# Kernel tuning notes

Measured on AMD Instinct MI355X. Metric: run time of the kernel, lower is better.

The kernel has to match this reference:

```python
import jax, jax.numpy as jnp
import numpy as np

N = 100_000      # nodes
E = 1_600_000    # directed input edges (no self loops, unique canonical pairs)
F_IN = 256       # num_features
HID = 128        # 2 * num_hidden (GATConv out width)
NHID = 64        # num_hidden
C = 4            # num_classes
G = 128          # number of graphs in the batch
NEG_SLOPE = 0.2  # PyG GATConv default LeakyReLU slope


def setup_inputs() -> dict:
    key = jax.random.key(0)
    ks = jax.random.split(key, 16)

    # --- graph structure (numpy; deduped canonical pairs so that
    # concat(e, reversed(e)) exactly matches PyG to_undirected+coalesce) ---
    rng = np.random.RandomState(0)
    n_cand = int(E * 1.05)
    s = rng.randint(0, N, size=n_cand)
    off = rng.randint(1, N, size=n_cand)
    d = (s + off) % N                      # guarantees no self loops
    lo, hi = np.minimum(s, d), np.maximum(s, d)
    pairs = np.unique(lo.astype(np.int64) * N + hi.astype(np.int64))[:E]
    src = (pairs // N).astype(np.int64)
    dst = (pairs % N).astype(np.int64)
    edge_index = jnp.asarray(np.stack([src, dst]))  # [2, E]

    batch = jnp.sort(jax.random.randint(ks[0], (N,), 0, G)).astype(jnp.int64)
    x = jax.random.normal(ks[1], (N, F_IN), dtype=jnp.float32)

    sc = 0.05
    params = dict(
        W1=jax.random.normal(ks[2], (HID, F_IN)) * sc,
        as1=jax.random.normal(ks[3], (HID,)) * sc,
        ad1=jax.random.normal(ks[4], (HID,)) * sc,
        b1=jnp.zeros((HID,), jnp.float32),
        W2=jax.random.normal(ks[5], (HID, HID)) * sc,
        as2=jax.random.normal(ks[6], (HID,)) * sc,
        ad2=jax.random.normal(ks[7], (HID,)) * sc,
        b2=jnp.zeros((HID,), jnp.float32),
        fw1=jax.random.normal(ks[8], (NHID, HID)) * sc,
        fb1=jnp.zeros((NHID,), jnp.float32),
        fw2=jax.random.normal(ks[9], (C, NHID)) * sc,
        fb2=jnp.zeros((C,), jnp.float32),
    )
    return dict(x=x, edge_index=edge_index, batch=batch, **params)


def _gat_conv(h_in, src, dst, W, a_src, a_dst, bias):
    """PyG GATConv, heads=1, concat=True. src/dst include self loops."""
    h = h_in @ W.T                                        # [N, out]
    # per-edge attention logits: a_src . h_j + a_dst . h_i
    e = jax.nn.leaky_relu((h @ a_src)[src] + (h @ a_dst)[dst], NEG_SLOPE)
    # edge softmax over incoming edges of each dst node
    m = jax.ops.segment_max(e, dst, num_segments=N)       # [N]
    w = jnp.exp(e - m[dst])
    denom = jax.ops.segment_sum(w, dst, num_segments=N)   # [N] (>0: self loops)
    alpha = w / denom[dst]                                # [Etot]
    out = jax.ops.segment_sum(h[src] * alpha[:, None], dst, num_segments=N)
    return out + bias


def reference(x, edge_index, batch,
              W1, as1, ad1, b1, W2, as2, ad2, b2,
              fw1, fb1, fw2, fb2):
    # to_undirected: input has unique canonical (lo<hi) pairs -> concat exact
    s0, d0 = edge_index[0], edge_index[1]
    loop = jnp.arange(N, dtype=s0.dtype)
    src = jnp.concatenate([s0, d0, loop])  # GATConv adds self loops
    dst = jnp.concatenate([d0, s0, loop])

    h = jax.nn.selu(_gat_conv(x, src, dst, W1, as1, ad1, b1))
    h = jax.nn.selu(_gat_conv(h, src, dst, W2, as2, ad2, b2))

    # global mean pool over graphs
    sums = jax.ops.segment_sum(h, batch, num_segments=G)            # [G, HID]
    cnt = jax.ops.segment_sum(jnp.ones((N,), h.dtype), batch, num_segments=G)
    g = jax.nn.selu(sums / jnp.maximum(cnt, 1.0)[:, None])

    g = jax.nn.selu(g @ fw1.T + fb1)
    # dropout p=0.5 is identity in eval mode
    logits = g @ fw2.T + fb2
    return jax.nn.log_softmax(logits, axis=-1)                      # [G, C]
```

## Files before the change

kernel.cpp:

```cpp
#include <hip/hip_runtime.h>
#include <hip/hip_bf16.h>


#define NN 100000
#define EE 1600000
#define GG 128
#define HID 128
#define AGG_CAP 512
#define NEG_SLOPE 0.2f

typedef short bf16x8 __attribute__((ext_vector_type(8)));
typedef float f32x4 __attribute__((ext_vector_type(4)));

__device__ __forceinline__ float lrelu(float x) { return x > 0.f ? x : NEG_SLOPE * x; }

__device__ __forceinline__ float selu(float x) {
    const float sc = 1.0507009873554805f, al = 1.6732632423543772f;
    return x > 0.f ? sc * x : sc * al * (__expf(x) - 1.f);
}

__device__ __forceinline__ unsigned short f2bf(float x) {
    unsigned int b = __float_as_uint(x);
    b += 0x7FFFu + ((b >> 16) & 1u);
    return (unsigned short)(b >> 16);
}


__global__ __launch_bounds__(256) void castbf_kernel(const float* __restrict__ in,
                                                     unsigned short* __restrict__ out, int n) {
    int i = (blockIdx.x * blockDim.x + threadIdx.x) * 4;
    if (i >= n) return;
    float4 v = *reinterpret_cast<const float4*>(in + i);
    union { unsigned short u[4]; uint2 w; } pk;
    pk.u[0] = f2bf(v.x); pk.u[1] = f2bf(v.y); pk.u[2] = f2bf(v.z); pk.u[3] = f2bf(v.w);
    *reinterpret_cast<uint2*>(out + i) = pk.w;
}


__global__ __launch_bounds__(256) void loptr_kernel(const int* __restrict__ ei,
                                                    int* __restrict__ loptr, int n, int E_) {
    int v = blockIdx.x * blockDim.x + threadIdx.x;
    if (v > n) return;
    int lo = 0, hi = E_;
    while (lo < hi) {
        int mid = (lo + hi) >> 1;
        if (ei[mid] < v) lo = mid + 1; else hi = mid;
    }
    loptr[v] = lo;
}


__global__ void count_kernel(const int* __restrict__ ei, int* __restrict__ deg, int E_) {
    int e = blockIdx.x * blockDim.x + threadIdx.x;
    if (e >= E_) return;
    atomicAdd(&deg[ei[E_ + e]], 1);
}

#define SCAN_CHUNK 512

__global__ __launch_bounds__(256) void block_sum_kernel(const int* __restrict__ deg,
                                                        int* __restrict__ bsum, int n) {
    __shared__ int sd[256];
    int b = blockIdx.x, t = threadIdx.x;
    int base = b * SCAN_CHUNK;
    int v = 0;
    int i0 = base + t, i1 = base + t + 256;
    if (i0 < n) v += deg[i0];
    if (i1 < n) v += deg[i1];
    sd[t] = v;
    __syncthreads();
    for (int off = 128; off; off >>= 1) {
        if (t < off) sd[t] += sd[t + off];
        __syncthreads();
    }
    if (t == 0) bsum[b] = sd[0];
}

__global__ __launch_bounds__(256) void top_scan_kernel(const int* __restrict__ bsum,
                                                       int* __restrict__ boff, int nb,
                                                       int* __restrict__ total_out) {
    __shared__ int a[256], b[256];
    int t = threadIdx.x;
    int v = (t < nb) ? bsum[t] : 0;
    int* cur = a; int* nxt = b;
    cur[t] = v;
    __syncthreads();
    for (int off = 1; off < 256; off <<= 1) {
        int val = cur[t] + ((t >= off) ? cur[t - off] : 0);
        nxt[t] = val;
        __syncthreads();
        int* tmp = cur; cur = nxt; nxt = tmp;
    }
    if (t < nb) boff[t] = cur[t] - v;
    if (t == nb - 1) *total_out = cur[t];
}

__global__ __launch_bounds__(512) void scan_final_kernel(const int* __restrict__ deg,
                                                         const int* __restrict__ boff,
                                                         int* __restrict__ row_ptr,
                                                         int* __restrict__ cursor, int n) {
    __shared__ int a[512], b[512];
    int blk = blockIdx.x, t = threadIdx.x;
    int i = blk * 512 + t;
    int v = (i < n) ? deg[i] : 0;
    int orig = v;
    int* cur = a; int* nxt = b;
    cur[t] = v;
    __syncthreads();
    for (int off = 1; off < 512; off <<= 1) {
        int val = cur[t] + ((t >= off) ? cur[t - off] : 0);
        nxt[t] = val;
        __syncthreads();
        int* tmp = cur; cur = nxt; nxt = tmp;
    }
    if (i < n) {
        int excl = cur[t] - orig + boff[blk];
        row_ptr[i] = excl;
        cursor[i] = excl;
    }
}

__global__ void scatter_kernel(const int* __restrict__ ei, int* __restrict__ cursor,
                               int* __restrict__ csr, int E_) {
    int e = blockIdx.x * blockDim.x + threadIdx.x;
    if (e >= E_) return;
    int u = ei[e], v = ei[E_ + e];
    int p = atomicAdd(&cursor[v], 1);
    csr[p] = u;
}


template<int K, bool BF16IN>
__global__ __launch_bounds__(256) void mfma_gemm(const void* __restrict__ Ain,
                                                 const unsigned short* __restrict__ Wb,
                                                 const float* __restrict__ avs,
                                                 const float* __restrict__ avd,
                                                 unsigned short* __restrict__ Cb,
                                                 float* __restrict__ hs,
                                                 float* __restrict__ hd,
                                                 int M) {
    __shared__ unsigned short As[128 * 32];
    __shared__ unsigned short Bs[128 * 32];
    __shared__ float hsp[128][2];
    __shared__ float hdp[128][2];
    int tid = threadIdx.x;
    int brow = blockIdx.x * 128;
    int w = tid >> 6, lane = tid & 63;
    int wr = (w >> 1) * 64, wc = (w & 1) * 64;
    int whalf = w & 1;
    int l15 = lane & 15, g = lane >> 4;

    const f32x4 zero = {0.f, 0.f, 0.f, 0.f};
    f32x4 acc[4][4];
    #pragma unroll
    for (int m = 0; m < 4; ++m)
        #pragma unroll
        for (int n = 0; n < 4; ++n) acc[m][n] = zero;

    int srow = tid >> 2;
    int slot = tid & 3;

    for (int k0 = 0; k0 < K; k0 += 32) {
        #pragma unroll
        for (int half = 0; half < 2; ++half) {
            int r = srow + half * 64;
            int grow = brow + r;
            union { unsigned short u[8]; uint4 v; } pk;
            if (BF16IN) {
                const unsigned short* A16 = (const unsigned short*)Ain;
                if (grow < M)
                    pk.v = *reinterpret_cast<const uint4*>(A16 + (size_t)grow * K + k0 + slot * 8);
                else pk.v = make_uint4(0, 0, 0, 0);
            } else {
                const float* A32 = (const float*)Ain;
                if (grow < M) {
                    const float4* p = reinterpret_cast<const float4*>(A32 + (size_t)grow * K + k0 + slot * 8);
                    float4 f0 = p[0], f1 = p[1];
                    pk.u[0] = f2bf(f0.x); pk.u[1] = f2bf(f0.y);
                    pk.u[2] = f2bf(f0.z); pk.u[3] = f2bf(f0.w);
                    pk.u[4] = f2bf(f1.x); pk.u[5] = f2bf(f1.y);
                    pk.u[6] = f2bf(f1.z); pk.u[7] = f2bf(f1.w);
                } else pk.v = make_uint4(0, 0, 0, 0);
            }
            int ss = slot ^ (r & 3);
            *reinterpret_cast<uint4*>(&As[r * 32 + ss * 8]) = pk.v;
        }
        #pragma unroll
        for (int half = 0; half < 2; ++half) {
            int r = srow + half * 64;
            uint4 v = *reinterpret_cast<const uint4*>(Wb + (size_t)r * K + k0 + slot * 8);
            int ss = slot ^ (r & 3);
            *reinterpret_cast<uint4*>(&Bs[r * 32 + ss * 8]) = v;
        }
        __syncthreads();

        bf16x8 af[4], bfr[4];
        #pragma unroll
        for (int m = 0; m < 4; ++m) {
            int row = wr + m * 16 + l15;
            af[m] = *reinterpret_cast<const bf16x8*>(&As[row * 32 + ((g ^ (row & 3)) * 8)]);
        }
        #pragma unroll
        for (int n = 0; n < 4; ++n) {
            int col = wc + n * 16 + l15;
            bfr[n] = *reinterpret_cast<const bf16x8*>(&Bs[col * 32 + ((g ^ (col & 3)) * 8)]);
        }
        #pragma unroll
        for (int m = 0; m < 4; ++m)
            #pragma unroll
            for (int n = 0; n < 4; ++n)
                acc[m][n] = __builtin_amdgcn_mfma_f32_16x16x32_bf16(af[m], bfr[n], acc[m][n], 0, 0, 0);
        __syncthreads();
    }

    #pragma unroll
    for (int m = 0; m < 4; ++m) {
        int rbase = brow + wr + m * 16 + g * 4;
        #pragma unroll
        for (int j = 0; j < 4; ++j) {
            int row = rbase + j;
            if (row < M) {
                #pragma unroll
                for (int n = 0; n < 4; ++n) {
                    int col = wc + n * 16 + l15;
                    Cb[(size_t)row * 128 + col] = f2bf(acc[m][n][j]);
                }
            }
        }
    }

    float asv[4], adv[4];
    #pragma unroll
    for (int n = 0; n < 4; ++n) {
        asv[n] = avs[wc + n * 16 + l15];
        adv[n] = avd[wc + n * 16 + l15];
    }
    #pragma unroll
    for (int m = 0; m < 4; ++m) {
        #pragma unroll
        for (int j = 0; j < 4; ++j) {
            float vs = 0.f, vd = 0.f;
            #pragma unroll
            for (int n = 0; n < 4; ++n) {
                float a = acc[m][n][j];
                vs = fmaf(a, asv[n], vs);
                vd = fmaf(a, adv[n], vd);
            }
            #pragma unroll
            for (int off = 1; off < 16; off <<= 1) {
                vs += __shfl_xor(vs, off);
                vd += __shfl_xor(vd, off);
            }
            if (l15 == 0) {
                int rl = wr + m * 16 + g * 4 + j;
                hsp[rl][whalf] = vs;
                hdp[rl][whalf] = vd;
            }
        }
    }
    __syncthreads();
    if (tid < 128) {
        int row = brow + tid;
        if (row < M) {
            hs[row] = hsp[tid][0] + hsp[tid][1];
            hd[row] = hdp[tid][0] + hdp[tid][1];
        }
    }
}


__global__ __launch_bounds__(256) void agg_kernel(const unsigned int* __restrict__ hb32,
                                                  const float* __restrict__ hs,
                                                  const float* __restrict__ hd,
                                                  const int* __restrict__ loptr,
                                                  const int* __restrict__ eiD,
                                                  const int* __restrict__ hiptr,
                                                  const int* __restrict__ csr,
                                                  const float* __restrict__ bias,
                                                  unsigned int* __restrict__ outb,
                                                  int n) {
    __shared__ float esh[4][AGG_CAP];
    __shared__ int ush[4][AGG_CAP];
    int wib = threadIdx.x >> 6;
    int lane = threadIdx.x & 63;
    int v = blockIdx.x * 4 + wib;
    if (v >= n) return;
    int s_lo = loptr[v];
    int dlo = loptr[v + 1] - s_lo;
    int s_hi = hiptr[v];
    int d = dlo + (hiptr[v + 1] - s_hi);
    float hdv = hd[v];
    float e_self = lrelu(hs[v] + hdv);
    float m, inv;
    bool fits = (d <= AGG_CAP);

    auto nbr = [&](int k) -> int {
        return (k < dlo) ? eiD[s_lo + k] : csr[s_hi + k - dlo];
    };
    auto gx = [&](int u) -> float2 {
        unsigned int w = hb32[(size_t)u * 64 + lane];
        return make_float2(__uint_as_float(w << 16), __uint_as_float(w & 0xFFFF0000u));
    };

    if (fits) {
        float mloc = -3.4e38f;
        for (int k = lane; k < d; k += 64) {
            int u = nbr(k);
            float e = lrelu(hs[u] + hdv);
            ush[wib][k] = u;
            esh[wib][k] = e;
            mloc = fmaxf(mloc, e);
        }
        #pragma unroll
        for (int off = 32; off; off >>= 1) mloc = fmaxf(mloc, __shfl_xor(mloc, off));
        m = fmaxf(mloc, e_self);
        float sloc = 0.f;
        for (int k = lane; k < d; k += 64) sloc += __expf(esh[wib][k] - m);
        #pragma unroll
        for (int off = 32; off; off >>= 1) sloc += __shfl_xor(sloc, off);
        float s = sloc + __expf(e_self - m);
        inv = 1.f / s;
        for (int k = lane; k < d; k += 64) esh[wib][k] = __expf(esh[wib][k] - m) * inv;
    } else {
        float mloc = -3.4e38f;
        for (int k = lane; k < d; k += 64) mloc = fmaxf(mloc, lrelu(hs[nbr(k)] + hdv));
        #pragma unroll
        for (int off = 32; off; off >>= 1) mloc = fmaxf(mloc, __shfl_xor(mloc, off));
        m = fmaxf(mloc, e_self);
        float sloc = 0.f;
        for (int k = lane; k < d; k += 64) sloc += __expf(lrelu(hs[nbr(k)] + hdv) - m);
        #pragma unroll
        for (int off = 32; off; off >>= 1) sloc += __shfl_xor(sloc, off);
        float s = sloc + __expf(e_self - m);
        inv = 1.f / s;
    }
    __syncthreads();

    float2 hvv = gx(v);
    float a_self = __expf(e_self - m) * inv;
    float accx = a_self * hvv.x;
    float accy = a_self * hvv.y;
    if (fits) {
        int k = 0;
        for (; k + 8 <= d; k += 8) {
            float a_[8]; int u_[8]; float2 x_[8];
            #pragma unroll
            for (int j = 0; j < 8; ++j) { a_[j] = esh[wib][k + j]; u_[j] = ush[wib][k + j]; }
            #pragma unroll
            for (int j = 0; j < 8; ++j) x_[j] = gx(u_[j]);
            #pragma unroll
            for (int j = 0; j < 8; ++j) {
                accx = fmaf(a_[j], x_[j].x, accx);
                accy = fmaf(a_[j], x_[j].y, accy);
            }
        }
        for (; k < d; ++k) {
            float al = esh[wib][k];
            float2 xv = gx(ush[wib][k]);
            accx = fmaf(al, xv.x, accx);
            accy = fmaf(al, xv.y, accy);
        }
    } else {
        for (int k = 0; k < d; ++k) {
            int u = nbr(k);
            float al = __expf(lrelu(hs[u] + hdv) - m) * inv;
            float2 xv = gx(u);
            accx = fmaf(al, xv.x, accx);
            accy = fmaf(al, xv.y, accy);
        }
    }
    float2 bb = reinterpret_cast<const float2*>(bias)[lane];
    float o0 = selu(accx + bb.x);
    float o1 = selu(accy + bb.y);
    unsigned int pb = ((unsigned int)f2bf(o1) << 16) | (unsigned int)f2bf(o0);
    outb[(size_t)v * 64 + lane] = pb;
}


__device__ __forceinline__ int lower_bound_dev(const int* __restrict__ b, int n, int val) {
    int lo = 0, hi = n;
    while (lo < hi) {
        int mid = (lo + hi) >> 1;
        if (b[mid] < val) lo = mid + 1; else hi = mid;
    }
    return lo;
}

__global__ __launch_bounds__(1024) void pool_mlp_kernel(const unsigned int* __restrict__ hb,
                                                        const int* __restrict__ batch,
                                                        const float* __restrict__ fw1,
                                                        const float* __restrict__ fb1,
                                                        const float* __restrict__ fw2,
                                                        const float* __restrict__ fb2,
                                                        float* __restrict__ out, int n) {
    int g = blockIdx.x;
    int t = threadIdx.x;
    int lane = t & 63;
    int rg = t >> 6;
    __shared__ float2 sm[16][64];
    __shared__ float gv[128];
    __shared__ float hid[64];
    __shared__ float logits[4];

    int s = lower_bound_dev(batch, n, g);
    int e = lower_bound_dev(batch, n, g + 1);

    float2 acc = make_float2(0.f, 0.f);
    int i = s + rg;
    for (; i + 16 < e; i += 32) {
        unsigned int w0 = hb[(size_t)i * 64 + lane];
        unsigned int w1 = hb[(size_t)(i + 16) * 64 + lane];
        acc.x += __uint_as_float(w0 << 16) + __uint_as_float(w1 << 16);
        acc.y += __uint_as_float(w0 & 0xFFFF0000u) + __uint_as_float(w1 & 0xFFFF0000u);
    }
    for (; i < e; i += 16) {
        unsigned int w0 = hb[(size_t)i * 64 + lane];
        acc.x += __uint_as_float(w0 << 16);
        acc.y += __uint_as_float(w0 & 0xFFFF0000u);
    }
    sm[rg][lane] = acc;
    __syncthreads();
    if (rg == 0) {
        float2 tot = make_float2(0.f, 0.f);
        #pragma unroll
        for (int r = 0; r < 16; ++r) {
            tot.x += sm[r][lane].x;
            tot.y += sm[r][lane].y;
        }
        float cnt = fmaxf((float)(e - s), 1.0f);
        gv[lane * 2 + 0] = selu(tot.x / cnt);
        gv[lane * 2 + 1] = selu(tot.y / cnt);
    }
    __syncthreads();
    if (t < 64) {
        float a = fb1[t];
        for (int k = 0; k < 128; ++k) a = fmaf(fw1[t * 128 + k], gv[k], a);
        hid[t] = selu(a);
    }
    __syncthreads();
    if (t < 4) {
        float a = fb2[t];
        for (int k = 0; k < 64; ++k) a = fmaf(fw2[t * 64 + k], hid[k], a);
        logits[t] = a;
    }
    __syncthreads();
    if (t < 4) {
        float mx = fmaxf(fmaxf(logits[0], logits[1]), fmaxf(logits[2], logits[3]));
        float sum = __expf(logits[0] - mx) + __expf(logits[1] - mx) +
                    __expf(logits[2] - mx) + __expf(logits[3] - mx);
        out[g * 4 + t] = logits[t] - mx - logf(sum);
    }
}


extern "C" void kernel_launch(void* const* d_in, const int* in_sizes, int n_in,
                              void* d_out, int out_size, void* d_ws, size_t ws_size,
                              hipStream_t stream) {
    const float* x   = (const float*)d_in[0];
    const int*   ei  = (const int*)d_in[1];
    const int*   bat = (const int*)d_in[2];
    const float* W1  = (const float*)d_in[3];
    const float* as1 = (const float*)d_in[4];
    const float* ad1 = (const float*)d_in[5];
    const float* b1  = (const float*)d_in[6];
    const float* W2  = (const float*)d_in[7];
    const float* as2 = (const float*)d_in[8];
    const float* ad2 = (const float*)d_in[9];
    const float* b2  = (const float*)d_in[10];
    const float* fw1 = (const float*)d_in[11];
    const float* fb1 = (const float*)d_in[12];
    const float* fw2 = (const float*)d_in[13];
    const float* fb2 = (const float*)d_in[14];
    float* out = (float*)d_out;

    char* ws = (char*)d_ws;
    size_t off = 0;
    auto alloc = [&](size_t bytes) {
        void* p = ws + off;
        off += (bytes + 255) & ~(size_t)255;
        return p;
    };
    unsigned short* hb      = (unsigned short*)alloc((size_t)NN * 128 * 2);
    unsigned short* hbB     = (unsigned short*)alloc((size_t)NN * 128 * 2);
    unsigned short* wb1     = (unsigned short*)alloc((size_t)HID * 256 * 2);
    unsigned short* wb2     = (unsigned short*)alloc((size_t)HID * 128 * 2);
    float*          hs      = (float*)alloc((size_t)NN * 4);
    float*          hd      = (float*)alloc((size_t)NN * 4);
    int*            deg     = (int*)alloc((size_t)NN * 4);
    int*            row_ptr = (int*)alloc((size_t)(NN + 1) * 4);
    int*            cursor  = (int*)alloc((size_t)NN * 4);
    int*            loptr   = (int*)alloc((size_t)(NN + 1) * 4);
    int*            csr     = (int*)alloc((size_t)EE * 4);
    int*            bsum    = (int*)alloc(256 * 4);
    int*            boff    = (int*)alloc(256 * 4);

    hipMemsetAsync(deg, 0, (size_t)NN * 4, stream);
    loptr_kernel<<<(NN + 1 + 255) / 256, 256, 0, stream>>>(ei, loptr, NN, EE);
    count_kernel<<<(EE + 255) / 256, 256, 0, stream>>>(ei, deg, EE);
    int NB = (NN + SCAN_CHUNK - 1) / SCAN_CHUNK;
    block_sum_kernel<<<NB, 256, 0, stream>>>(deg, bsum, NN);
    top_scan_kernel<<<1, 256, 0, stream>>>(bsum, boff, NB, row_ptr + NN);
    scan_final_kernel<<<NB, 512, 0, stream>>>(deg, boff, row_ptr, cursor, NN);
    scatter_kernel<<<(EE + 255) / 256, 256, 0, stream>>>(ei, cursor, csr, EE);

    castbf_kernel<<<(HID * 256 / 4 + 255) / 256, 256, 0, stream>>>(W1, wb1, HID * 256);
    castbf_kernel<<<(HID * 128 / 4 + 255) / 256, 256, 0, stream>>>(W2, wb2, HID * 128);

    const int* eiD = ei + EE;
    int gemmGrid = (NN + 127) / 128;

    mfma_gemm<256, false><<<gemmGrid, 256, 0, stream>>>(x, wb1, as1, ad1, hb, hs, hd, NN);
    agg_kernel<<<(NN + 3) / 4, 256, 0, stream>>>((const unsigned int*)hb, hs, hd,
                                                 loptr, eiD, row_ptr, csr, b1,
                                                 (unsigned int*)hbB, NN);

    mfma_gemm<128, true><<<gemmGrid, 256, 0, stream>>>(hbB, wb2, as2, ad2, hb, hs, hd, NN);
    agg_kernel<<<(NN + 3) / 4, 256, 0, stream>>>((const unsigned int*)hb, hs, hd,
                                                 loptr, eiD, row_ptr, csr, b2,
                                                 (unsigned int*)hbB, NN);

    pool_mlp_kernel<<<GG, 1024, 0, stream>>>((const unsigned int*)hbB, bat,
                                             fw1, fb1, fw2, fb2, out, NN);
}
```

Measured before the change: 682.9 us.

## Build CSR via two-pass bucketed partition instead of global atomic scatter

Replaces the global-atomic scatter CSR build with a two-pass radix-style partition. Edges are first histogrammed per workgroup into 256-node buckets, scanned, and written into a bucketed temp array. Each bucket is then locally sorted in LDS and written out contiguously. The loptr binary search is also replaced by an adjacent-difference fill over edges. The aim is to cut contended global atomics and random writes, at the cost of more kernel launches and an extra 8-byte-per-edge temp buffer pass.

```diff
diff --git a/kernel.cpp b/kernel.cpp
--- a/kernel.cpp
+++ b/kernel.cpp
@@ -8,6 +8,12 @@
 #define HID 128
 #define AGG_CAP 512
 #define NEG_SLOPE 0.2f
+
+#define NWG1 256
+#define CHUNK1 (EE / NWG1)
+#define BSH2 8
+#define NBKT2 ((NN + 255) >> 8)
+#define P2CAP 16384
 
 typedef short bf16x8 __attribute__((ext_vector_type(8)));
 typedef float f32x4 __attribute__((ext_vector_type(4)));
@@ -37,16 +43,15 @@
 }
 
 
-__global__ __launch_bounds__(256) void loptr_kernel(const int* __restrict__ ei,
-                                                    int* __restrict__ loptr, int n, int E_) {
-    int v = blockIdx.x * blockDim.x + threadIdx.x;
-    if (v > n) return;
-    int lo = 0, hi = E_;
-    while (lo < hi) {
-        int mid = (lo + hi) >> 1;
-        if (ei[mid] < v) lo = mid + 1; else hi = mid;
-    }
-    loptr[v] = lo;
+__global__ __launch_bounds__(256) void loptr_fill(const int* __restrict__ ei,
+                                                  int* __restrict__ loptr, int n, int E_) {
+    int e = blockIdx.x * blockDim.x + threadIdx.x;
+    if (e >= E_) return;
+    int cur = ei[e];
+    int prev = (e == 0) ? -1 : ei[e - 1];
+    for (int v = prev + 1; v <= cur; ++v) loptr[v] = e;
+    if (e == E_ - 1)
+        for (int v = cur + 1; v <= n; ++v) loptr[v] = E_;
 }
 
 
@@ -97,8 +102,7 @@
 
 __global__ __launch_bounds__(512) void scan_final_kernel(const int* __restrict__ deg,
                                                          const int* __restrict__ boff,
-                                                         int* __restrict__ row_ptr,
-                                                         int* __restrict__ cursor, int n) {
+                                                         int* __restrict__ row_ptr, int n) {
     __shared__ int a[512], b[512];
     int blk = blockIdx.x, t = threadIdx.x;
     int i = blk * 512 + t;
@@ -113,20 +117,85 @@
         __syncthreads();
         int* tmp = cur; cur = nxt; nxt = tmp;
     }
-    if (i < n) {
-        int excl = cur[t] - orig + boff[blk];
-        row_ptr[i] = excl;
-        cursor[i] = excl;
-    }
-}
-
-__global__ void scatter_kernel(const int* __restrict__ ei, int* __restrict__ cursor,
-                               int* __restrict__ csr, int E_) {
-    int e = blockIdx.x * blockDim.x + threadIdx.x;
-    if (e >= E_) return;
-    int u = ei[e], v = ei[E_ + e];
-    int p = atomicAdd(&cursor[v], 1);
-    csr[p] = u;
+    if (i < n) row_ptr[i] = cur[t] - orig + boff[blk];
+}
+
+
+__global__ __launch_bounds__(256) void part_hist(const int* __restrict__ ei,
+                                                 int* __restrict__ histG) {
+    __shared__ int hist[NBKT2];
+    int wg = blockIdx.x, t = threadIdx.x;
+    for (int i = t; i < NBKT2; i += 256) hist[i] = 0;
+    __syncthreads();
+    int s = wg * CHUNK1;
+    for (int e = s + t; e < s + CHUNK1; e += 256)
+        atomicAdd(&hist[ei[EE + e] >> BSH2], 1);
+    __syncthreads();
+    for (int i = t; i < NBKT2; i += 256) histG[wg * NBKT2 + i] = hist[i];
+}
+
+__global__ __launch_bounds__(256) void part_scan(const int* __restrict__ histG,
+                                                 const int* __restrict__ row_ptr,
+                                                 int* __restrict__ baseG) {
+    __shared__ int a[256], b[256];
+    int tbk = blockIdx.x, w = threadIdx.x;
+    int v = histG[w * NBKT2 + tbk];
+    int orig = v;
+    int* cur = a; int* nxt = b;
+    cur[w] = v;
+    __syncthreads();
+    for (int off = 1; off < 256; off <<= 1) {
+        int val = cur[w] + ((w >= off) ? cur[w - off] : 0);
+        nxt[w] = val;
+        __syncthreads();
+        int* tp = cur; cur = nxt; nxt = tp;
+    }
+    baseG[w * NBKT2 + tbk] = row_ptr[tbk << BSH2] + cur[w] - orig;
+}
+
+__global__ __launch_bounds__(256) void part_write(const int* __restrict__ ei,
+                                                  const int* __restrict__ baseG,
+                                                  uint2* __restrict__ tmp) {
+    __shared__ int cur[NBKT2];
+    int wg = blockIdx.x, t = threadIdx.x;
+    for (int i = t; i < NBKT2; i += 256) cur[i] = baseG[wg * NBKT2 + i];
+    __syncthreads();
+    int s = wg * CHUNK1;
+    for (int e = s + t; e < s + CHUNK1; e += 256) {
+        int u = ei[e], v = ei[EE + e];
+        int p = atomicAdd(&cur[v >> BSH2], 1);
+        tmp[p] = make_uint2((unsigned)u, (unsigned)v);
+    }
+}
+
+__global__ __launch_bounds__(256) void pass2_kernel(const uint2* __restrict__ tmp,
+                                                    const int* __restrict__ row_ptr,
+                                                    int* __restrict__ csr, int n) {
+    __shared__ int lcur[256];
+    __shared__ int outb[P2CAP];
+    int t = blockIdx.x, tid = threadIdx.x;
+    int nodebase = t << BSH2;
+    int ncnt = min(256, n - nodebase);
+    int gstart = row_ptr[nodebase];
+    int gend = row_ptr[min(nodebase + 256, n)];
+    int len = gend - gstart;
+    if (tid < ncnt) lcur[tid] = row_ptr[nodebase + tid] - gstart;
+    __syncthreads();
+    if (len <= P2CAP) {
+        for (int i = tid; i < len; i += 256) {
+            uint2 e = tmp[gstart + i];
+            int lp = atomicAdd(&lcur[(int)e.y - nodebase], 1);
+            outb[lp] = (int)e.x;
+        }
+        __syncthreads();
+        for (int i = tid; i < len; i += 256) csr[gstart + i] = outb[i];
+    } else {
+        for (int i = tid; i < len; i += 256) {
+            uint2 e = tmp[gstart + i];
+            int lp = atomicAdd(&lcur[(int)e.y - nodebase], 1);
+            csr[gstart + lp] = (int)e.x;
+        }
+    }
 }
 
 
@@ -488,20 +557,25 @@
     float*          hd      = (float*)alloc((size_t)NN * 4);
     int*            deg     = (int*)alloc((size_t)NN * 4);
     int*            row_ptr = (int*)alloc((size_t)(NN + 1) * 4);
-    int*            cursor  = (int*)alloc((size_t)NN * 4);
     int*            loptr   = (int*)alloc((size_t)(NN + 1) * 4);
     int*            csr     = (int*)alloc((size_t)EE * 4);
+    uint2*          tmp     = (uint2*)alloc((size_t)EE * 8);
+    int*            histG   = (int*)alloc((size_t)NWG1 * NBKT2 * 4);
+    int*            baseG   = (int*)alloc((size_t)NWG1 * NBKT2 * 4);
     int*            bsum    = (int*)alloc(256 * 4);
     int*            boff    = (int*)alloc(256 * 4);
 
     hipMemsetAsync(deg, 0, (size_t)NN * 4, stream);
-    loptr_kernel<<<(NN + 1 + 255) / 256, 256, 0, stream>>>(ei, loptr, NN, EE);
+    loptr_fill<<<(EE + 255) / 256, 256, 0, stream>>>(ei, loptr, NN, EE);
     count_kernel<<<(EE + 255) / 256, 256, 0, stream>>>(ei, deg, EE);
     int NB = (NN + SCAN_CHUNK - 1) / SCAN_CHUNK;
     block_sum_kernel<<<NB, 256, 0, stream>>>(deg, bsum, NN);
     top_scan_kernel<<<1, 256, 0, stream>>>(bsum, boff, NB, row_ptr + NN);
-    scan_final_kernel<<<NB, 512, 0, stream>>>(deg, boff, row_ptr, cursor, NN);
-    scatter_kernel<<<(EE + 255) / 256, 256, 0, stream>>>(ei, cursor, csr, EE);
+    scan_final_kernel<<<NB, 512, 0, stream>>>(deg, boff, row_ptr, NN);
+    part_hist<<<NWG1, 256, 0, stream>>>(ei, histG);
+    part_scan<<<NBKT2, 256, 0, stream>>>(histG, row_ptr, baseG);
+    part_write<<<NWG1, 256, 0, stream>>>(ei, baseG, tmp);
+    pass2_kernel<<<NBKT2, 256, 0, stream>>>(tmp, row_ptr, csr, NN);
 
     castbf_kernel<<<(HID * 256 / 4 + 255) / 256, 256, 0, stream>>>(W1, wb1, HID * 256);
     castbf_kernel<<<(HID * 128 / 4 + 255) / 256, 256, 0, stream>>>(W2, wb2, HID * 128);
```

Result: slower. 978.1 us (+43.2%).
